# Optimization experiments

Hardware: AMD Instinct MI355X
Metric: run time of the kernel (lower is better)

The kernel has to match this reference:

```python
import jax, jax.numpy as jnp
import numpy as np

B, S, D, H = 2, 1024, 1024, 16
DH = D // H


def setup_inputs() -> dict:
    key = jax.random.key(0)
    k1, k2, k3 = jax.random.split(key, 3)
    x = jax.random.normal(k1, (B, S, D), dtype=jnp.float32)
    # nn.Linear weight layout: [out_features, in_features]; scaled for stable softmax logits
    W_qkv = jax.random.normal(k2, (3 * D, D), dtype=jnp.float32) * 0.02
    W_out = jax.random.normal(k3, (D, D), dtype=jnp.float32) * 0.02
    return {"x": x, "W_qkv": W_qkv, "W_out": W_out}


def reference(x, W_qkv, W_out):
    Bx, Sx, Dx = x.shape
    # fused QKV projection: [B,S,3D]
    qkv = jnp.einsum('bsd,ed->bse', x, W_qkv)
    qkv = qkv.reshape(Bx, Sx, 3, H, DH)
    q, k, v = jnp.moveaxis(qkv, 2, 0).transpose(0, 1, 3, 2, 4)
    scale = 1.0 / jnp.sqrt(jnp.asarray(DH, dtype=x.dtype))
    scores = jnp.einsum('bhqd,bhkd->bhqk', q, k) * scale  # [B,H,S,S]
    attn = jax.nn.softmax(scores, axis=-1)
    out = jnp.einsum('bhqk,bhkd->bhqd', attn, v)  # [B,H,S,DH]
    out = out.transpose(0, 2, 1, 3).reshape(Bx, Sx, Dx)  # [B,S,D]
    return jnp.einsum('bsd,ed->bse', out, W_out)
```

## Files before the change

kernel.cpp:

```cpp
#include <hip/hip_runtime.h>

#define B_  2
#define S_  1024
#define D_  1024
#define H_  16
#define DH_ 64

typedef __attribute__((ext_vector_type(8))) short bf16x8;
typedef __attribute__((ext_vector_type(4))) float f32x4;

__device__ __forceinline__ unsigned short f2bf(float f) {
  unsigned int u = __float_as_uint(f);
  u += 0x7fff + ((u >> 16) & 1);
  return (unsigned short)(u >> 16);
}

__device__ __forceinline__ unsigned int pack2bf(float a, float b) {
  return (unsigned int)f2bf(a) | ((unsigned int)f2bf(b) << 16);
}

__device__ __forceinline__ void gload_lds16(const void* g, void* l) {
  __builtin_amdgcn_global_load_lds(
      (const __attribute__((address_space(1))) unsigned int*)g,
      (__attribute__((address_space(3))) unsigned int*)l, 16, 0, 0);
}

__global__ __launch_bounds__(256)
void cvt_kernel(const float4* __restrict__ x, const float4* __restrict__ wq,
                const float4* __restrict__ wo, unsigned short* __restrict__ xb,
                unsigned short* __restrict__ wqb, unsigned short* __restrict__ wob) {
  constexpr int n1 = (B_*S_*D_) / 4;
  constexpr int n2 = (3*D_*D_) / 4;
  constexpr int n3 = (D_*D_) / 4;
  for (int i = blockIdx.x*blockDim.x + threadIdx.x; i < n1+n2+n3;
       i += gridDim.x*blockDim.x) {
    const float4* src; unsigned short* dst; int off;
    if (i < n1)          { src = x;  dst = xb;  off = i; }
    else if (i < n1+n2)  { src = wq; dst = wqb; off = i - n1; }
    else                 { src = wo; dst = wob; off = i - n1 - n2; }
    float4 v = src[off];
    ushort4 r;
    r.x = f2bf(v.x); r.y = f2bf(v.y); r.z = f2bf(v.z); r.w = f2bf(v.w);
    *(ushort4*)&dst[off*4] = r;
  }
}

template<int M, int N, int K, int EPI>
__global__ __launch_bounds__(256)
void gemm_bt(const unsigned short* __restrict__ A, const unsigned short* __restrict__ Bw,
             float* __restrict__ C, unsigned short* __restrict__ Qb,
             unsigned short* __restrict__ Kb, unsigned short* __restrict__ Vtb) {
  constexpr int NBN = N / 128;
  __shared__ unsigned short As[128*32];
  __shared__ unsigned short Bs[128*32];
  const int tid = threadIdx.x;
  const int bid = blockIdx.x;
  const int mb = bid / NBN, nb = bid % NBN;
  const int wid = tid >> 6, lane = tid & 63;
  const int wr = wid >> 1, wc = wid & 1;
  const int lg = lane >> 4, lr = lane & 15;

  f32x4 acc[4][4] = {};

  const int mrow = mb*128, nrow = nb*128;
  const int srow = tid >> 2;
  const int scol = (tid & 3) * 8;

  for (int k0 = 0; k0 < K; k0 += 32) {
    #pragma unroll
    for (int h = 0; h < 2; ++h) {
      gload_lds16(A  + (size_t)(mrow + h*64 + srow)*K + k0 + scol, &As[(h*256 + tid)*8]);
      gload_lds16(Bw + (size_t)(nrow + h*64 + srow)*K + k0 + scol, &Bs[(h*256 + tid)*8]);
    }
    __syncthreads();
    bf16x8 af[4], bfr[4];
    #pragma unroll
    for (int t = 0; t < 4; ++t) {
      af[t]  = *(const bf16x8*)&As[(wr*64 + t*16 + lr)*32 + lg*8];
      bfr[t] = *(const bf16x8*)&Bs[(wc*64 + t*16 + lr)*32 + lg*8];
    }
    #pragma unroll
    for (int mt = 0; mt < 4; ++mt)
      #pragma unroll
      for (int nt = 0; nt < 4; ++nt)
        acc[mt][nt] = __builtin_amdgcn_mfma_f32_16x16x32_bf16(af[mt], bfr[nt], acc[mt][nt], 0, 0, 0);
    __syncthreads();
  }

  #pragma unroll
  for (int mt = 0; mt < 4; ++mt) {
    const int m0 = mrow + wr*64 + mt*16 + lg*4;
    #pragma unroll
    for (int nt = 0; nt < 4; ++nt) {
      const int n = nrow + wc*64 + nt*16 + lr;
      f32x4 v = acc[mt][nt];
      if constexpr (EPI == 0) {
        #pragma unroll
        for (int i = 0; i < 4; ++i) C[(size_t)(m0 + i)*N + n] = v[i];
      } else {
        const int t3 = n >> 10, rem = n & 1023;
        const int hh = rem >> 6, dh = rem & 63;
        const int b = m0 >> 10, s0 = m0 & 1023;
        if (t3 == 2) {
          ushort4 pk;
          pk.x = f2bf(v[0]); pk.y = f2bf(v[1]); pk.z = f2bf(v[2]); pk.w = f2bf(v[3]);
          *(ushort4*)&Vtb[(size_t)((b*H_ + hh)*DH_ + dh)*S_ + s0] = pk;
        } else {
          unsigned short* dst = (t3 == 0) ? Qb : Kb;
          #pragma unroll
          for (int i = 0; i < 4; ++i)
            dst[(size_t)((b*H_ + hh)*S_ + s0 + i)*DH_ + dh] = f2bf(v[i]);
        }
      }
    }
  }
}

__global__ __launch_bounds__(512, 2)
void attn_kernel(const unsigned short* __restrict__ Qb, const unsigned short* __restrict__ Kb,
                 const unsigned short* __restrict__ Vtb, unsigned short* __restrict__ AOb) {
  __shared__ unsigned short Ks[2][64*64];
  __shared__ unsigned short Vs[2][64*64];
  __shared__ unsigned short Pl[8][16*72];
  const int bid = blockIdx.x;
  const int xcd = bid & 7, rr = bid >> 3;
  const int qt = rr & 7;
  const int bh = (rr >> 3) * 8 + xcd;
  const int tid = threadIdx.x, wid = tid >> 6, lane = tid & 63;
  const int lg = lane >> 4, lr = lane & 15;
  const unsigned short* Q  = Qb  + (size_t)bh*S_*DH_;
  const unsigned short* Kp = Kb  + (size_t)bh*S_*DH_;
  const unsigned short* Vt = Vtb + (size_t)bh*DH_*S_;
  const int q0 = qt*128 + wid*16;

  bf16x8 qf0 = *(const bf16x8*)&Q[(size_t)(q0 + lr)*DH_ + lg*8];
  bf16x8 qf1 = *(const bf16x8*)&Q[(size_t)(q0 + lr)*DH_ + 32 + lg*8];

  const int sr = tid >> 3;
  const int gc = (tid & 7) ^ (sr & 7);

  float mrun = -1e30f, lrun = 0.f;
  f32x4 o[4] = {};
  const int rsw = lr & 7;

  gload_lds16(Kp + (size_t)sr*DH_ + gc*8,  &Ks[0][tid*8]);
  gload_lds16(Vt + (size_t)sr*S_  + gc*8,  &Vs[0][tid*8]);
  __syncthreads();

  int buf = 0;
  for (int t = 0; t < 16; ++t) {
    const int jn = (t + 1) * 64;
    if (t < 15) {
      gload_lds16(Kp + (size_t)(jn + sr)*DH_ + gc*8, &Ks[buf^1][tid*8]);
      gload_lds16(Vt + (size_t)sr*S_ + jn + gc*8,    &Vs[buf^1][tid*8]);
    }
    f32x4 sv[4];
    #pragma unroll
    for (int f = 0; f < 4; ++f) {
      bf16x8 ka = *(const bf16x8*)&Ks[buf][(16*f + lr)*64 + ((lg     ^ rsw)*8)];
      bf16x8 kb = *(const bf16x8*)&Ks[buf][(16*f + lr)*64 + (((lg+4) ^ rsw)*8)];
      f32x4 z = {};
      z     = __builtin_amdgcn_mfma_f32_16x16x32_bf16(ka, qf0, z, 0, 0, 0);
      sv[f] = __builtin_amdgcn_mfma_f32_16x16x32_bf16(kb, qf1, z, 0, 0, 0);
    }
    float s[16];
    #pragma unroll
    for (int f = 0; f < 4; ++f)
      #pragma unroll
      for (int i = 0; i < 4; ++i) s[4*f + i] = sv[f][i] * 0.125f;
    float t8[8];
    #pragma unroll
    for (int k = 0; k < 8; ++k) t8[k] = fmaxf(s[k], s[k+8]);
    float t4a = fmaxf(t8[0], t8[4]), t4b = fmaxf(t8[1], t8[5]);
    float t4c = fmaxf(t8[2], t8[6]), t4d = fmaxf(t8[3], t8[7]);
    float pmax = fmaxf(fmaxf(t4a, t4b), fmaxf(t4c, t4d));
    pmax = fmaxf(pmax, __shfl_xor(pmax, 16));
    pmax = fmaxf(pmax, __shfl_xor(pmax, 32));
    float mnew = fmaxf(mrun, pmax);
    float cr = __expf(mrun - mnew);
    float p[16];
    #pragma unroll
    for (int k = 0; k < 16; ++k) p[k] = __expf(s[k] - mnew);
    float u8[8];
    #pragma unroll
    for (int k = 0; k < 8; ++k) u8[k] = p[k] + p[k+8];
    float u4a = u8[0]+u8[4], u4b = u8[1]+u8[5], u4c = u8[2]+u8[6], u4d = u8[3]+u8[7];
    float rs = (u4a + u4b) + (u4c + u4d);
    rs += __shfl_xor(rs, 16);
    rs += __shfl_xor(rs, 32);
    lrun = lrun*cr + rs;
    mrun = mnew;
    #pragma unroll
    for (int f = 0; f < 4; ++f) {
      uint2 w;
      w.x = pack2bf(p[4*f],   p[4*f+1]);
      w.y = pack2bf(p[4*f+2], p[4*f+3]);
      *(uint2*)&Pl[wid][lr*72 + f*16 + lg*4] = w;
    }
    #pragma unroll
    for (int dt = 0; dt < 4; ++dt) {
      o[dt][0] *= cr; o[dt][1] *= cr; o[dt][2] *= cr; o[dt][3] *= cr;
    }
    asm volatile("s_waitcnt lgkmcnt(0)" ::: "memory");
    #pragma unroll
    for (int c = 0; c < 2; ++c) {
      bf16x8 pf = *(const bf16x8*)&Pl[wid][lr*72 + c*32 + lg*8];
      #pragma unroll
      for (int dt = 0; dt < 4; ++dt) {
        bf16x8 vfr = *(const bf16x8*)&Vs[buf][(dt*16 + lr)*64 + (((c*4 + lg) ^ rsw)*8)];
        o[dt] = __builtin_amdgcn_mfma_f32_16x16x32_bf16(vfr, pf, o[dt], 0, 0, 0);
      }
    }
    __syncthreads();
    buf ^= 1;
  }

  const float inv = 1.0f / lrun;
  const int b = bh >> 4, hh = bh & 15;
  #pragma unroll
  for (int dt = 0; dt < 4; ++dt) {
    ushort4 pk;
    pk.x = f2bf(o[dt][0]*inv); pk.y = f2bf(o[dt][1]*inv);
    pk.z = f2bf(o[dt][2]*inv); pk.w = f2bf(o[dt][3]*inv);
    *(ushort4*)&AOb[(size_t)(b*S_ + q0 + lr)*D_ + hh*DH_ + dt*16 + lg*4] = pk;
  }
}

extern "C" void kernel_launch(void* const* d_in, const int* in_sizes, int n_in,
                              void* d_out, int out_size, void* d_ws, size_t ws_size,
                              hipStream_t stream) {
  const float* x  = (const float*)d_in[0];
  const float* wq = (const float*)d_in[1];
  const float* wo = (const float*)d_in[2];
  float* out = (float*)d_out;

  unsigned short* w = (unsigned short*)d_ws;
  unsigned short* xb  = w;
  unsigned short* wqb = xb  + 2097152;
  unsigned short* wob = wqb + 3145728;
  unsigned short* qb  = wob + 1048576;
  unsigned short* kb  = qb  + 2097152;
  unsigned short* vtb = kb  + 2097152;
  unsigned short* aob = vtb + 2097152;

  cvt_kernel<<<dim3(1024), dim3(256), 0, stream>>>(
      (const float4*)x, (const float4*)wq, (const float4*)wo, xb, wqb, wob);

  gemm_bt<2048, 3072, 1024, 1><<<dim3(16*24), dim3(256), 0, stream>>>(
      xb, wqb, nullptr, qb, kb, vtb);

  attn_kernel<<<dim3(256), dim3(512), 0, stream>>>(qb, kb, vtb, aob);

  gemm_bt<2048, 1024, 1024, 0><<<dim3(16*8), dim3(256), 0, stream>>>(
      aob, wob, out, nullptr, nullptr, nullptr);
}
```

Measured before the change: 146.5 us.

## Shrink GEMM M-tiles and attention blocks to raise grid size; add MFMA priority hints

```diff
diff --git a/kernel.cpp b/kernel.cpp
--- a/kernel.cpp
+++ b/kernel.cpp
@@ -45,13 +45,15 @@
   }
 }
 
-template<int M, int N, int K, int EPI>
+template<int BM, int M, int N, int K, int EPI>
 __global__ __launch_bounds__(256)
 void gemm_bt(const unsigned short* __restrict__ A, const unsigned short* __restrict__ Bw,
              float* __restrict__ C, unsigned short* __restrict__ Qb,
              unsigned short* __restrict__ Kb, unsigned short* __restrict__ Vtb) {
   constexpr int NBN = N / 128;
-  __shared__ unsigned short As[128*32];
+  constexpr int MT  = BM / 32;
+  constexpr int AH  = BM / 64;
+  __shared__ unsigned short As[BM*32];
   __shared__ unsigned short Bs[128*32];
   const int tid = threadIdx.x;
   const int bid = blockIdx.x;
@@ -60,36 +62,38 @@
   const int wr = wid >> 1, wc = wid & 1;
   const int lg = lane >> 4, lr = lane & 15;
 
-  f32x4 acc[4][4] = {};
-
-  const int mrow = mb*128, nrow = nb*128;
+  f32x4 acc[MT][4] = {};
+
+  const int mrow = mb*BM, nrow = nb*128;
   const int srow = tid >> 2;
   const int scol = (tid & 3) * 8;
 
   for (int k0 = 0; k0 < K; k0 += 32) {
     #pragma unroll
-    for (int h = 0; h < 2; ++h) {
+    for (int h = 0; h < AH; ++h)
       gload_lds16(A  + (size_t)(mrow + h*64 + srow)*K + k0 + scol, &As[(h*256 + tid)*8]);
+    #pragma unroll
+    for (int h = 0; h < 2; ++h)
       gload_lds16(Bw + (size_t)(nrow + h*64 + srow)*K + k0 + scol, &Bs[(h*256 + tid)*8]);
-    }
     __syncthreads();
-    bf16x8 af[4], bfr[4];
-    #pragma unroll
-    for (int t = 0; t < 4; ++t) {
-      af[t]  = *(const bf16x8*)&As[(wr*64 + t*16 + lr)*32 + lg*8];
-      bfr[t] = *(const bf16x8*)&Bs[(wc*64 + t*16 + lr)*32 + lg*8];
-    }
-    #pragma unroll
-    for (int mt = 0; mt < 4; ++mt)
+    bf16x8 af[MT], bfr[4];
+    #pragma unroll
+    for (int m = 0; m < MT; ++m)
+      af[m]  = *(const bf16x8*)&As[(wr*(BM/2) + m*16 + lr)*32 + lg*8];
+    #pragma unroll
+    for (int n = 0; n < 4; ++n)
+      bfr[n] = *(const bf16x8*)&Bs[(wc*64 + n*16 + lr)*32 + lg*8];
+    #pragma unroll
+    for (int m = 0; m < MT; ++m)
       #pragma unroll
-      for (int nt = 0; nt < 4; ++nt)
-        acc[mt][nt] = __builtin_amdgcn_mfma_f32_16x16x32_bf16(af[mt], bfr[nt], acc[mt][nt], 0, 0, 0);
+      for (int n = 0; n < 4; ++n)
+        acc[m][n] = __builtin_amdgcn_mfma_f32_16x16x32_bf16(af[m], bfr[n], acc[m][n], 0, 0, 0);
     __syncthreads();
   }
 
   #pragma unroll
-  for (int mt = 0; mt < 4; ++mt) {
-    const int m0 = mrow + wr*64 + mt*16 + lg*4;
+  for (int mt = 0; mt < MT; ++mt) {
+    const int m0 = mrow + wr*(BM/2) + mt*16 + lg*4;
     #pragma unroll
     for (int nt = 0; nt < 4; ++nt) {
       const int n = nrow + wc*64 + nt*16 + lr;
@@ -116,45 +120,50 @@
   }
 }
 
-__global__ __launch_bounds__(512, 2)
+__global__ __launch_bounds__(256, 2)
 void attn_kernel(const unsigned short* __restrict__ Qb, const unsigned short* __restrict__ Kb,
                  const unsigned short* __restrict__ Vtb, unsigned short* __restrict__ AOb) {
   __shared__ unsigned short Ks[2][64*64];
   __shared__ unsigned short Vs[2][64*64];
-  __shared__ unsigned short Pl[8][16*72];
+  __shared__ unsigned short Pl[4][16*72];
   const int bid = blockIdx.x;
   const int xcd = bid & 7, rr = bid >> 3;
-  const int qt = rr & 7;
-  const int bh = (rr >> 3) * 8 + xcd;
+  const int qt = rr & 15;
+  const int bh = (rr >> 4) * 8 + xcd;
   const int tid = threadIdx.x, wid = tid >> 6, lane = tid & 63;
   const int lg = lane >> 4, lr = lane & 15;
   const unsigned short* Q  = Qb  + (size_t)bh*S_*DH_;
   const unsigned short* Kp = Kb  + (size_t)bh*S_*DH_;
   const unsigned short* Vt = Vtb + (size_t)bh*DH_*S_;
-  const int q0 = qt*128 + wid*16;
+  const int q0 = qt*64 + wid*16;
 
   bf16x8 qf0 = *(const bf16x8*)&Q[(size_t)(q0 + lr)*DH_ + lg*8];
   bf16x8 qf1 = *(const bf16x8*)&Q[(size_t)(q0 + lr)*DH_ + 32 + lg*8];
 
   const int sr = tid >> 3;
-  const int gc = (tid & 7) ^ (sr & 7);
+  const int g0 = (tid & 7) ^ (sr & 7);
 
   float mrun = -1e30f, lrun = 0.f;
   f32x4 o[4] = {};
   const int rsw = lr & 7;
 
-  gload_lds16(Kp + (size_t)sr*DH_ + gc*8,  &Ks[0][tid*8]);
-  gload_lds16(Vt + (size_t)sr*S_  + gc*8,  &Vs[0][tid*8]);
+  gload_lds16(Kp + (size_t)sr*DH_        + g0*8, &Ks[0][tid*8]);
+  gload_lds16(Kp + (size_t)(sr+32)*DH_   + g0*8, &Ks[0][(256+tid)*8]);
+  gload_lds16(Vt + (size_t)sr*S_         + g0*8, &Vs[0][tid*8]);
+  gload_lds16(Vt + (size_t)(sr+32)*S_    + g0*8, &Vs[0][(256+tid)*8]);
   __syncthreads();
 
   int buf = 0;
   for (int t = 0; t < 16; ++t) {
     const int jn = (t + 1) * 64;
     if (t < 15) {
-      gload_lds16(Kp + (size_t)(jn + sr)*DH_ + gc*8, &Ks[buf^1][tid*8]);
-      gload_lds16(Vt + (size_t)sr*S_ + jn + gc*8,    &Vs[buf^1][tid*8]);
+      gload_lds16(Kp + (size_t)(jn + sr)*DH_      + g0*8, &Ks[buf^1][tid*8]);
+      gload_lds16(Kp + (size_t)(jn + sr + 32)*DH_ + g0*8, &Ks[buf^1][(256+tid)*8]);
+      gload_lds16(Vt + (size_t)sr*S_      + jn + g0*8,    &Vs[buf^1][tid*8]);
+      gload_lds16(Vt + (size_t)(sr+32)*S_ + jn + g0*8,    &Vs[buf^1][(256+tid)*8]);
     }
     f32x4 sv[4];
+    __builtin_amdgcn_s_setprio(1);
     #pragma unroll
     for (int f = 0; f < 4; ++f) {
       bf16x8 ka = *(const bf16x8*)&Ks[buf][(16*f + lr)*64 + ((lg     ^ rsw)*8)];
@@ -163,6 +172,7 @@
       z     = __builtin_amdgcn_mfma_f32_16x16x32_bf16(ka, qf0, z, 0, 0, 0);
       sv[f] = __builtin_amdgcn_mfma_f32_16x16x32_bf16(kb, qf1, z, 0, 0, 0);
     }
+    __builtin_amdgcn_s_setprio(0);
     float s[16];
     #pragma unroll
     for (int f = 0; f < 4; ++f)
@@ -202,6 +212,7 @@
       o[dt][0] *= cr; o[dt][1] *= cr; o[dt][2] *= cr; o[dt][3] *= cr;
     }
     asm volatile("s_waitcnt lgkmcnt(0)" ::: "memory");
+    __builtin_amdgcn_s_setprio(1);
     #pragma unroll
     for (int c = 0; c < 2; ++c) {
       bf16x8 pf = *(const bf16x8*)&Pl[wid][lr*72 + c*32 + lg*8];
@@ -211,6 +222,7 @@
         o[dt] = __builtin_amdgcn_mfma_f32_16x16x32_bf16(vfr, pf, o[dt], 0, 0, 0);
       }
     }
+    __builtin_amdgcn_s_setprio(0);
     __syncthreads();
     buf ^= 1;
   }
@@ -246,11 +258,11 @@
   cvt_kernel<<<dim3(1024), dim3(256), 0, stream>>>(
       (const float4*)x, (const float4*)wq, (const float4*)wo, xb, wqb, wob);
 
-  gemm_bt<2048, 3072, 1024, 1><<<dim3(16*24), dim3(256), 0, stream>>>(
+  gemm_bt<64, 2048, 3072, 1024, 1><<<dim3(32*24), dim3(256), 0, stream>>>(
       xb, wqb, nullptr, qb, kb, vtb);
 
-  attn_kernel<<<dim3(256), dim3(512), 0, stream>>>(qb, kb, vtb, aob);
-
-  gemm_bt<2048, 1024, 1024, 0><<<dim3(16*8), dim3(256), 0, stream>>>(
+  attn_kernel<<<dim3(512), dim3(256), 0, stream>>>(qb, kb, vtb, aob);
+
+  gemm_bt<64, 2048, 1024, 1024, 0><<<dim3(32*8), dim3(256), 0, stream>>>(
       aob, wob, out, nullptr, nullptr, nullptr);
 }
```

Measured after the change: 141.6 us. 1.03x faster.
